# Kernel tuning notes

Measured on AMD Instinct MI355X. Metric: run time of the kernel, lower is better.

The kernel has to match this reference:

```python
import jax, jax.numpy as jnp
import numpy as np

# SplineConv (PyG), dim=1, kernel_size=2, degree=1, open spline, aggr='mean',
# root_weight=True, bias=True.
# For K=2, m=1, dim=1 the B-spline basis per edge reduces exactly to
#   basis = (1 - u, u) with kernel indices (0, 1), u = edge_attr[:, 0] in [0, 1].

N_NODES = 50000
N_EDGES = 1600000
D_IN = 128
D_OUT = 128


def setup_inputs() -> dict:
    key = jax.random.key(0)
    k1, k2, k3, k4, k5, k6, k7 = jax.random.split(key, 7)
    x = jax.random.normal(k1, (N_NODES, D_IN), dtype=jnp.float32)
    edge_index = jax.random.randint(k2, (2, N_EDGES), 0, N_NODES, dtype=jnp.int64)
    edge_attr = jax.random.uniform(k3, (N_EDGES, 1), dtype=jnp.float32)
    # Glorot-ish init for spline weights [K^dim=2, D_IN, D_OUT]
    scale = 1.0 / np.sqrt(D_IN)
    W = jax.random.normal(k4, (2, D_IN, D_OUT), dtype=jnp.float32) * scale
    W_root = jax.random.normal(k5, (D_IN, D_OUT), dtype=jnp.float32) * scale
    bias = jax.random.normal(k6, (D_OUT,), dtype=jnp.float32) * 0.01
    return {"x": x, "edge_index": edge_index, "edge_attr": edge_attr,
            "W": W, "W_root": W_root, "bias": bias}


def reference(x, edge_index, edge_attr, W, W_root, bias):
    n = x.shape[0]
    src, dst = edge_index[0], edge_index[1]
    u = jnp.clip(edge_attr[:, 0], 0.0, 1.0)          # [E]
    # Node-level GEMMs for both kernel weight slots (cheaper than per-edge GEMM)
    h = jnp.einsum('nd,kde->kne', x, W)              # [2, N, D_OUT]
    # Per-edge spline-weighted message: (1-u)*h0[src] + u*h1[src]
    msg = (1.0 - u)[:, None] * h[0][src] + u[:, None] * h[1][src]  # [E, D_OUT]
    agg = jax.ops.segment_sum(msg, dst, num_segments=n)            # [N, D_OUT]
    deg = jax.ops.segment_sum(jnp.ones_like(u), dst, num_segments=n)
    agg = agg / jnp.maximum(deg, 1.0)[:, None]       # mean aggregation
    return agg + x @ W_root + bias
```

## Files before the change

kernel.cpp:

```cpp
#include <hip/hip_runtime.h>

static constexpr int N = 50000;
static constexpr int E = 1600000;
static constexpr int D = 128;
static constexpr int NB = (N + 63) / 64;
static constexpr int BIN_BLKS = 512;
static constexpr int CHUNK = E / BIN_BLKS;
static constexpr int BKT_CAP = 3072;
static constexpr int CVT_BLKS = (N * D / 8 + 1023) / 1024;
static constexpr int W_BLKS = 48;

typedef __attribute__((ext_vector_type(8))) short short8;
typedef __attribute__((ext_vector_type(4))) float f32x4;
typedef __attribute__((ext_vector_type(2))) float f32x2;

__device__ __forceinline__ uint bf16rne2(float a, float b) {
    uint ua = __float_as_uint(a), ub = __float_as_uint(b);
    ua += 0x7fffu + ((ua >> 16) & 1u);
    ub += 0x7fffu + ((ub >> 16) & 1u);
    return (ua >> 16) | (ub & 0xffff0000u);
}

__device__ __forceinline__ int logical_blk() {
    return (blockIdx.x & 7) * (BIN_BLKS / 8) + (blockIdx.x >> 3);
}

__global__ __launch_bounds__(1024) void binprep_k(
        const int* __restrict__ ei, const float* __restrict__ ea,
        const float* __restrict__ x, const float* __restrict__ W,
        const float* __restrict__ Wr, int* __restrict__ gcur,
        uint* __restrict__ pay, ushort* __restrict__ xb,
        uchar* __restrict__ xf8, ushort* __restrict__ Wt) {
    __shared__ int hist[NB];
    __shared__ int base[NB];
    int t = threadIdx.x;
    if (blockIdx.x < BIN_BLKS) {
        int b = logical_blk();
        for (int j = t; j < NB; j += 1024) hist[j] = 0;
        __syncthreads();
        int b0 = b * CHUNK;
        for (int i = b0 + t; i < b0 + CHUNK; i += 1024) {
            int dst = ei[E + i];
            if ((unsigned)dst < (unsigned)N) atomicAdd(&hist[dst >> 6], 1);
        }
        __syncthreads();
        for (int j = t; j < NB; j += 1024) {
            int c = hist[j];
            base[j] = c ? atomicAdd(&gcur[j], c) : 0;
            hist[j] = 0;
        }
        __syncthreads();
        for (int i = b0 + t; i < b0 + CHUNK; i += 1024) {
            int dst = ei[E + i];
            if ((unsigned)dst >= (unsigned)N) continue;
            int src = ei[i];
            float u = fminf(fmaxf(ea[i], 0.0f), 1.0f);
            uint u10 = (uint)(u * 1023.0f + 0.5f);
            int bkt = dst >> 6;
            int r = atomicAdd(&hist[bkt], 1);
            int pos = base[bkt] + r;
            if (pos < BKT_CAP)
                pay[(size_t)bkt * BKT_CAP + pos] =
                    (u10 << 22) | ((uint)(dst & 63) << 16) | (uint)src;
        }
    } else if (blockIdx.x < BIN_BLKS + CVT_BLKS) {
        int i = (blockIdx.x - BIN_BLKS) * 1024 + t;
        if (i < N * D / 8) {
            float4 v0 = ((const float4*)x)[2 * i];
            float4 v1 = ((const float4*)x)[2 * i + 1];
            uint4 ob = { bf16rne2(v0.x, v0.y), bf16rne2(v0.z, v0.w),
                         bf16rne2(v1.x, v1.y), bf16rne2(v1.z, v1.w) };
            ((uint4*)xb)[i] = ob;
            int lo = __builtin_amdgcn_cvt_pk_fp8_f32(v0.x, v0.y, 0, false);
            lo = __builtin_amdgcn_cvt_pk_fp8_f32(v0.z, v0.w, lo, true);
            int hi = __builtin_amdgcn_cvt_pk_fp8_f32(v1.x, v1.y, 0, false);
            hi = __builtin_amdgcn_cvt_pk_fp8_f32(v1.z, v1.w, hi, true);
            uint2 o8 = { (uint)lo, (uint)hi };
            ((uint2*)xf8)[i] = o8;
        }
    } else {
        int i = (blockIdx.x - BIN_BLKS - CVT_BLKS) * 1024 + t;
        int n = i / 384, r = i % 384;
        float v = (r < 256) ? W[(size_t)r * 128 + n]
                            : Wr[(size_t)(r - 256) * 128 + n];
        uint u = __float_as_uint(v);
        u += 0x7fffu + ((u >> 16) & 1u);
        Wt[(size_t)n * 384 + r] = (ushort)(u >> 16);
    }
}

__global__ __launch_bounds__(1024) void sortagg_k(
        const uchar* __restrict__ xf8, const int* __restrict__ gcur,
        const uint* __restrict__ pay, ushort* __restrict__ a0b,
        ushort* __restrict__ a1b) {
    __shared__ uint srt[BKT_CAP];
    __shared__ int hist[64];
    __shared__ int off64[65];
    int b = blockIdx.x, t = threadIdx.x;
    int beg = b * BKT_CAP;
    int c = gcur[b];
    if (c > BKT_CAP) c = BKT_CAP;
    if (t < 64) hist[t] = 0;
    __syncthreads();
    uint mypay[3]; int myrank[3];
#pragma unroll
    for (int k = 0; k < 3; ++k) {
        int i = t + k * 1024;
        if (i < c) {
            uint p = pay[beg + i];
            mypay[k] = p;
            myrank[k] = atomicAdd(&hist[(p >> 16) & 63], 1);
        }
    }
    __syncthreads();
    if (t < 64) {
        int v = hist[t];
        int s = v;
        for (int d = 1; d < 64; d <<= 1) {
            int o = __shfl_up(s, d);
            if (t >= d) s += o;
        }
        off64[t] = s - v;
        if (t == 63) off64[64] = s;
    }
    __syncthreads();
#pragma unroll
    for (int k = 0; k < 3; ++k) {
        int i = t + k * 1024;
        if (i < c) {
            uint p = mypay[k];
            srt[off64[(p >> 16) & 63] + myrank[k]] = p;
        }
    }
    __syncthreads();

    int lane = t & 63;
    int wv   = t >> 6;
    int grp  = (lane >> 4);
    int cl   = lane & 15;
    int nloc = wv * 4 + grp;
    int s0 = off64[nloc], s1 = off64[nloc + 1];
    int deg = s1 - s0;

    f32x2 S[4], T[4];
#pragma unroll
    for (int q = 0; q < 4; ++q) { S[q] = 0.f; T[q] = 0.f; }

    int j = s0;
    for (; j + 3 < s1; j += 4) {
        uint p[4];
        uint2 v[4];
#pragma unroll
        for (int d = 0; d < 4; ++d) p[d] = srt[j + d];
#pragma unroll
        for (int d = 0; d < 4; ++d)
            v[d] = *(const uint2*)(xf8 + (size_t)(p[d] & 0xffffu) * D + cl * 8);
#pragma unroll
        for (int d = 0; d < 4; ++d) {
            float u = (float)(p[d] >> 22) * (1.0f / 1023.0f);
            f32x2 u2 = {u, u};
            f32x2 xv0 = __builtin_amdgcn_cvt_pk_f32_fp8((int)v[d].x, false);
            f32x2 xv1 = __builtin_amdgcn_cvt_pk_f32_fp8((int)v[d].x, true);
            f32x2 xv2 = __builtin_amdgcn_cvt_pk_f32_fp8((int)v[d].y, false);
            f32x2 xv3 = __builtin_amdgcn_cvt_pk_f32_fp8((int)v[d].y, true);
            S[0] += xv0; T[0] = u2 * xv0 + T[0];
            S[1] += xv1; T[1] = u2 * xv1 + T[1];
            S[2] += xv2; T[2] = u2 * xv2 + T[2];
            S[3] += xv3; T[3] = u2 * xv3 + T[3];
        }
    }
    for (; j < s1; ++j) {
        uint p0 = srt[j];
        uint2 v0 = *(const uint2*)(xf8 + (size_t)(p0 & 0xffffu) * D + cl * 8);
        float u = (float)(p0 >> 22) * (1.0f / 1023.0f);
        f32x2 u2 = {u, u};
        f32x2 xv0 = __builtin_amdgcn_cvt_pk_f32_fp8((int)v0.x, false);
        f32x2 xv1 = __builtin_amdgcn_cvt_pk_f32_fp8((int)v0.x, true);
        f32x2 xv2 = __builtin_amdgcn_cvt_pk_f32_fp8((int)v0.y, false);
        f32x2 xv3 = __builtin_amdgcn_cvt_pk_f32_fp8((int)v0.y, true);
        S[0] += xv0; T[0] = u2 * xv0 + T[0];
        S[1] += xv1; T[1] = u2 * xv1 + T[1];
        S[2] += xv2; T[2] = u2 * xv2 + T[2];
        S[3] += xv3; T[3] = u2 * xv3 + T[3];
    }

    int node = b * 64 + nloc;
    if (node < N) {
        float inv = 1.0f / fmaxf((float)deg, 1.0f);
        uint4 oa = { bf16rne2((S[0].x - T[0].x) * inv, (S[0].y - T[0].y) * inv),
                     bf16rne2((S[1].x - T[1].x) * inv, (S[1].y - T[1].y) * inv),
                     bf16rne2((S[2].x - T[2].x) * inv, (S[2].y - T[2].y) * inv),
                     bf16rne2((S[3].x - T[3].x) * inv, (S[3].y - T[3].y) * inv) };
        uint4 ob = { bf16rne2(T[0].x * inv, T[0].y * inv),
                     bf16rne2(T[1].x * inv, T[1].y * inv),
                     bf16rne2(T[2].x * inv, T[2].y * inv),
                     bf16rne2(T[3].x * inv, T[3].y * inv) };
        *(uint4*)(a0b + (size_t)node * D + cl * 8) = oa;
        *(uint4*)(a1b + (size_t)node * D + cl * 8) = ob;
    }
}

__global__ __launch_bounds__(256) void gemm_k(
        const ushort* __restrict__ a0b, const ushort* __restrict__ a1b,
        const ushort* __restrict__ xb, const ushort* __restrict__ Wt,
        const float* __restrict__ bias, float* __restrict__ out) {
    constexpr int LST = 40;
    __shared__ ushort As[128 * LST];
    __shared__ ushort Bs[128 * LST];

    int t    = threadIdx.x;
    int lane = t & 63;
    int w    = t >> 6;
    int r2   = w >> 1, c2 = w & 1;
    int q    = lane >> 4;
    int l16  = lane & 15;
    int row0 = blockIdx.x * 128;

    f32x4 acc[4][4];
#pragma unroll
    for (int i = 0; i < 4; ++i)
#pragma unroll
        for (int j = 0; j < 4; ++j) acc[i][j] = 0.f;

    const ushort* Asrc[3] = {a0b, a1b, xb};

    for (int kt = 0; kt < 384; kt += 32) {
        const ushort* Ab = Asrc[kt >> 7];
        int ko = kt & 127;
#pragma unroll
        for (int h = 0; h < 2; ++h) {
            int s  = t + h * 256;
            int r  = s >> 2;
            int q4 = s & 3;
            int rg = row0 + r;
            uint4 av = make_uint4(0, 0, 0, 0);
            if (rg < N) av = *(const uint4*)(Ab + (size_t)rg * 128 + ko + q4 * 8);
            *(uint4*)&As[r * LST + q4 * 8] = av;
            uint4 bv = *(const uint4*)(Wt + (size_t)r * 384 + kt + q4 * 8);
            *(uint4*)&Bs[r * LST + q4 * 8] = bv;
        }
        __syncthreads();
        short8 af[4], bf[4];
#pragma unroll
        for (int mt = 0; mt < 4; ++mt)
            af[mt] = *(const short8*)&As[(r2 * 64 + mt * 16 + l16) * LST + q * 8];
#pragma unroll
        for (int nt = 0; nt < 4; ++nt)
            bf[nt] = *(const short8*)&Bs[(c2 * 64 + nt * 16 + l16) * LST + q * 8];
#pragma unroll
        for (int mt = 0; mt < 4; ++mt)
#pragma unroll
            for (int nt = 0; nt < 4; ++nt)
                acc[mt][nt] = __builtin_amdgcn_mfma_f32_16x16x32_bf16(
                    af[mt], bf[nt], acc[mt][nt], 0, 0, 0);
        __syncthreads();
    }

#pragma unroll
    for (int nt = 0; nt < 4; ++nt) {
        int col = c2 * 64 + nt * 16 + l16;
        float bb = bias[col];
#pragma unroll
        for (int mt = 0; mt < 4; ++mt) {
#pragma unroll
            for (int r = 0; r < 4; ++r) {
                int row = row0 + r2 * 64 + mt * 16 + q * 4 + r;
                if (row < N) out[(size_t)row * 128 + col] = acc[mt][nt][r] + bb;
            }
        }
    }
}

extern "C" void kernel_launch(void* const* d_in, const int* in_sizes, int n_in,
                              void* d_out, int out_size, void* d_ws, size_t ws_size,
                              hipStream_t stream) {
    const float* x    = (const float*)d_in[0];
    const int*   ei   = (const int*)d_in[1];
    const float* ea   = (const float*)d_in[2];
    const float* W    = (const float*)d_in[3];
    const float* Wr   = (const float*)d_in[4];
    const float* bias = (const float*)d_in[5];
    float* out = (float*)d_out;

    char* ws = (char*)d_ws;
    size_t o = 0;
    auto alloc = [&](size_t bytes) -> void* {
        void* p = ws + o;
        o = (o + bytes + 255) & ~(size_t)255;
        return p;
    };
    int*    gcur = (int*)alloc((size_t)NB * 4);
    uint*   pay  = (uint*)alloc((size_t)NB * BKT_CAP * 4);
    ushort* xb   = (ushort*)alloc((size_t)N * D * 2);
    uchar*  xf8  = (uchar*)alloc((size_t)N * D);
    ushort* a0b  = (ushort*)alloc((size_t)N * D * 2);
    ushort* a1b  = (ushort*)alloc((size_t)N * D * 2);
    ushort* Wt   = (ushort*)alloc((size_t)128 * 384 * 2);
    (void)ws_size; (void)in_sizes; (void)n_in; (void)out_size;

    hipMemsetAsync(gcur, 0, (size_t)NB * 4, stream);
    binprep_k<<<BIN_BLKS + CVT_BLKS + W_BLKS, 1024, 0, stream>>>(
                 ei, ea, x, W, Wr, gcur, pay, xb, xf8, Wt);
    sortagg_k<<<NB, 1024, 0, stream>>>(xf8, gcur, pay, a0b, a1b);
    gemm_k   <<<(N + 127) / 128, 256, 0, stream>>>(a0b, a1b, xb, Wt, bias, out);
}
```

Baseline: 176.6 us.

## Single-pass register-cached edge binning and direct-to-LDS swizzled GEMM tile loads

The binning stage now reads each edge once, keeps its packed payload, bucket and rank in registers, and scatters after the global base reservation. The old code read the edge list twice, and halving the bin block count means each thread carries more slots. The GEMM now uses global_load_lds 16-byte async loads into an XOR-swizzled LDS layout with a K-step of 64, which halves the barrier count and avoids bank conflicts. In exchange, register pressure in binprep rises, the launch has fewer blocks, and out-of-range rows are clamped instead of zero-filled.

```diff
diff --git a/kernel.cpp b/kernel.cpp
--- a/kernel.cpp
+++ b/kernel.cpp
@@ -4,8 +4,9 @@
 static constexpr int E = 1600000;
 static constexpr int D = 128;
 static constexpr int NB = (N + 63) / 64;
-static constexpr int BIN_BLKS = 512;
+static constexpr int BIN_BLKS = 256;
 static constexpr int CHUNK = E / BIN_BLKS;
+static constexpr int SLOTS = (CHUNK + 1023) / 1024;
 static constexpr int BKT_CAP = 3072;
 static constexpr int CVT_BLKS = (N * D / 8 + 1023) / 1024;
 static constexpr int W_BLKS = 48;
@@ -19,6 +20,12 @@
     ua += 0x7fffu + ((ua >> 16) & 1u);
     ub += 0x7fffu + ((ub >> 16) & 1u);
     return (ua >> 16) | (ub & 0xffff0000u);
+}
+
+__device__ __forceinline__ void gload16(const void* g, void* l) {
+    __builtin_amdgcn_global_load_lds(
+        (const __attribute__((address_space(1))) void*)g,
+        (__attribute__((address_space(3))) void*)l, 16, 0, 0);
 }
 
 __device__ __forceinline__ int logical_blk() {
@@ -39,29 +46,39 @@
         for (int j = t; j < NB; j += 1024) hist[j] = 0;
         __syncthreads();
         int b0 = b * CHUNK;
-        for (int i = b0 + t; i < b0 + CHUNK; i += 1024) {
-            int dst = ei[E + i];
-            if ((unsigned)dst < (unsigned)N) atomicAdd(&hist[dst >> 6], 1);
+        uint mypay[SLOTS];
+        int  mybkt[SLOTS];
+        int  myrank[SLOTS];
+#pragma unroll
+        for (int k = 0; k < SLOTS; ++k) {
+            int i = b0 + t + k * 1024;
+            myrank[k] = -1;
+            if (t + k * 1024 < CHUNK) {
+                int dst = ei[E + i];
+                if ((unsigned)dst < (unsigned)N) {
+                    int src = ei[i];
+                    float u = fminf(fmaxf(ea[i], 0.0f), 1.0f);
+                    uint u10 = (uint)(u * 1023.0f + 0.5f);
+                    int bkt = dst >> 6;
+                    mybkt[k] = bkt;
+                    mypay[k] = (u10 << 22) | ((uint)(dst & 63) << 16) | (uint)src;
+                    myrank[k] = atomicAdd(&hist[bkt], 1);
+                }
+            }
         }
         __syncthreads();
         for (int j = t; j < NB; j += 1024) {
             int c = hist[j];
             base[j] = c ? atomicAdd(&gcur[j], c) : 0;
-            hist[j] = 0;
-        }
-        __syncthreads();
-        for (int i = b0 + t; i < b0 + CHUNK; i += 1024) {
-            int dst = ei[E + i];
-            if ((unsigned)dst >= (unsigned)N) continue;
-            int src = ei[i];
-            float u = fminf(fmaxf(ea[i], 0.0f), 1.0f);
-            uint u10 = (uint)(u * 1023.0f + 0.5f);
-            int bkt = dst >> 6;
-            int r = atomicAdd(&hist[bkt], 1);
-            int pos = base[bkt] + r;
-            if (pos < BKT_CAP)
-                pay[(size_t)bkt * BKT_CAP + pos] =
-                    (u10 << 22) | ((uint)(dst & 63) << 16) | (uint)src;
+        }
+        __syncthreads();
+#pragma unroll
+        for (int k = 0; k < SLOTS; ++k) {
+            if (myrank[k] >= 0) {
+                int pos = base[mybkt[k]] + myrank[k];
+                if (pos < BKT_CAP)
+                    pay[(size_t)mybkt[k] * BKT_CAP + pos] = mypay[k];
+            }
         }
     } else if (blockIdx.x < BIN_BLKS + CVT_BLKS) {
         int i = (blockIdx.x - BIN_BLKS) * 1024 + t;
@@ -204,9 +221,8 @@
         const ushort* __restrict__ a0b, const ushort* __restrict__ a1b,
         const ushort* __restrict__ xb, const ushort* __restrict__ Wt,
         const float* __restrict__ bias, float* __restrict__ out) {
-    constexpr int LST = 40;
-    __shared__ ushort As[128 * LST];
-    __shared__ ushort Bs[128 * LST];
+    __shared__ ushort As[128 * 64];
+    __shared__ ushort Bs[128 * 64];
 
     int t    = threadIdx.x;
     int lane = t & 63;
@@ -215,6 +231,9 @@
     int q    = lane >> 4;
     int l16  = lane & 15;
     int row0 = blockIdx.x * 128;
+    int rsub  = lane >> 3;
+    int cslot = lane & 7;
+    int xorc  = cslot ^ rsub;
 
     f32x4 acc[4][4];
 #pragma unroll
@@ -224,35 +243,41 @@
 
     const ushort* Asrc[3] = {a0b, a1b, xb};
 
-    for (int kt = 0; kt < 384; kt += 32) {
+#pragma unroll
+    for (int kt = 0; kt < 384; kt += 64) {
         const ushort* Ab = Asrc[kt >> 7];
         int ko = kt & 127;
 #pragma unroll
-        for (int h = 0; h < 2; ++h) {
-            int s  = t + h * 256;
-            int r  = s >> 2;
-            int q4 = s & 3;
-            int rg = row0 + r;
-            uint4 av = make_uint4(0, 0, 0, 0);
-            if (rg < N) av = *(const uint4*)(Ab + (size_t)rg * 128 + ko + q4 * 8);
-            *(uint4*)&As[r * LST + q4 * 8] = av;
-            uint4 bv = *(const uint4*)(Wt + (size_t)r * 384 + kt + q4 * 8);
-            *(uint4*)&Bs[r * LST + q4 * 8] = bv;
-        }
-        __syncthreads();
-        short8 af[4], bf[4];
-#pragma unroll
-        for (int mt = 0; mt < 4; ++mt)
-            af[mt] = *(const short8*)&As[(r2 * 64 + mt * 16 + l16) * LST + q * 8];
-#pragma unroll
-        for (int nt = 0; nt < 4; ++nt)
-            bf[nt] = *(const short8*)&Bs[(c2 * 64 + nt * 16 + l16) * LST + q * 8];
-#pragma unroll
-        for (int mt = 0; mt < 4; ++mt)
-#pragma unroll
-            for (int nt = 0; nt < 4; ++nt)
-                acc[mt][nt] = __builtin_amdgcn_mfma_f32_16x16x32_bf16(
-                    af[mt], bf[nt], acc[mt][nt], 0, 0, 0);
+        for (int h = 0; h < 4; ++h) {
+            int region = h * 4 + w;
+            int r = region * 8 + rsub;
+            int ra = row0 + r; ra = ra < N ? ra : N - 1;
+            gload16(Ab + (size_t)ra * 128 + ko + xorc * 8, As + region * 512);
+            gload16(Wt + (size_t)r * 384 + kt + xorc * 8,  Bs + region * 512);
+        }
+        __syncthreads();
+#pragma unroll
+        for (int kk = 0; kk < 2; ++kk) {
+            short8 af[4], bf[4];
+#pragma unroll
+            for (int mt = 0; mt < 4; ++mt) {
+                int r = r2 * 64 + mt * 16 + l16;
+                int slot = (kk * 4 + q) ^ (r & 7);
+                af[mt] = *(const short8*)&As[r * 64 + slot * 8];
+            }
+#pragma unroll
+            for (int nt = 0; nt < 4; ++nt) {
+                int n = c2 * 64 + nt * 16 + l16;
+                int slot = (kk * 4 + q) ^ (n & 7);
+                bf[nt] = *(const short8*)&Bs[n * 64 + slot * 8];
+            }
+#pragma unroll
+            for (int mt = 0; mt < 4; ++mt)
+#pragma unroll
+                for (int nt = 0; nt < 4; ++nt)
+                    acc[mt][nt] = __builtin_amdgcn_mfma_f32_16x16x32_bf16(
+                        af[mt], bf[nt], acc[mt][nt], 0, 0, 0);
+        }
         __syncthreads();
     }
 
```

New measurement: 161.2 us. -8.7%, faster.
